# Kernel tuning notes

Hardware: AMD Instinct MI355X
Metric: run time of the kernel (lower is better)

## Reference

```python
import jax, jax.numpy as jnp
import numpy as np

WEIGHT_GROUP = 128  # in-channel group size for scales (module default)


def setup_inputs() -> dict:
    key = jax.random.key(0)
    k1, k2, k3, k4, k5 = jax.random.split(key, 5)
    B, IN, OUT = 16, 8192, 8192
    nG = IN // WEIGHT_GROUP  # 64 scale groups along in_features
    x = jax.random.normal(k1, (B, IN), dtype=jnp.float32)
    # 'weight' stores the already-quantized low-bit float values (small magnitudes)
    weight = jax.random.normal(k2, (OUT, IN), dtype=jnp.float32)
    # per-(row, group) positive scales
    scale_buf = jax.random.uniform(k3, (OUT, nG), dtype=jnp.float32, minval=0.01, maxval=1.0)
    bias = jax.random.normal(k4, (1, OUT), dtype=jnp.float32)
    # per-[64, group]-block mantissa-format ids in {0,1,2}; selects the dequant
    # format on hardware but is a constant lookup (no float math) in the reference
    types = jax.random.randint(k5, (OUT // 64, nG), 0, 3, dtype=jnp.int32)
    return {"x": x, "weight": weight, "scale_buf": scale_buf, "bias": bias, "types": types}


def reference(x, weight, scale_buf, bias, types):
    O, I = weight.shape
    nG = scale_buf.shape[1]
    G = I // nG
    # group-wise dequant: w_deq[o, g*G + j] = weight[o, g*G + j] * scale_buf[o, g]
    w_deq = (weight.reshape(O, nG, G) * scale_buf[:, :, None]).reshape(O, I)
    # y = x @ W_deq^T + bias   [B, O]
    return jnp.einsum("bi,oi->bo", x, w_deq) + bias
```

## Files before the change

### kernel.cpp

```cpp
#include <hip/hip_runtime.h>

#define IN_F 8192
#define OUT_F 8192
#define NBATCH 16
#define KC 512
#define NG 64

__global__ __launch_bounds__(256, 2)
void axcore_dsew_linear_kernel(const float* __restrict__ x,
                               const float* __restrict__ w,
                               const float* __restrict__ scale,
                               const float* __restrict__ bias,
                               float* __restrict__ out) {
    __shared__ __align__(16) float xlds[NBATCH * KC];

    const int t    = threadIdx.x;
    const int wv   = t >> 6;
    const int lane = t & 63;
    const int o0   = blockIdx.x * 16 + wv * 4;

    float acc[4][16];
#pragma unroll
    for (int r = 0; r < 4; ++r)
#pragma unroll
        for (int b = 0; b < NBATCH; ++b) acc[r][b] = 0.f;

    for (int kc = 0; kc < IN_F; kc += KC) {
        __syncthreads();
#pragma unroll
        for (int p = 0; p < 8; ++p) {
            const int fidx = p * 256 + t;
            const int bb = fidx >> 7;
            const int kq = fidx & 127;
            const float4 v = *(const float4*)&x[bb * IN_F + kc + 4 * kq];
            *(float4*)&xlds[bb * KC + 4 * kq] = v;
        }
        __syncthreads();

        float4 scq[4];
#pragma unroll
        for (int r = 0; r < 4; ++r)
            scq[r] = *(const float4*)&scale[(o0 + r) * NG + (kc >> 7)];

#pragma unroll
        for (int s = 0; s < 2; ++s) {
            const int klocal = s * 256 + 4 * lane;
            const int kg = kc + klocal;

            float4 wq[4];
#pragma unroll
            for (int r = 0; r < 4; ++r)
                wq[r] = *(const float4*)&w[(size_t)(o0 + r) * IN_F + kg];

#pragma unroll
            for (int r = 0; r < 4; ++r) {
                float sr;
                if (s == 0) sr = (lane < 32) ? scq[r].x : scq[r].y;
                else        sr = (lane < 32) ? scq[r].z : scq[r].w;
                wq[r].x *= sr; wq[r].y *= sr; wq[r].z *= sr; wq[r].w *= sr;
            }

#pragma unroll
            for (int b = 0; b < NBATCH; ++b) {
                const float4 xv = *(const float4*)&xlds[b * KC + klocal];
#pragma unroll
                for (int r = 0; r < 4; ++r) {
                    acc[r][b] += wq[r].x * xv.x;
                    acc[r][b] += wq[r].y * xv.y;
                    acc[r][b] += wq[r].z * xv.z;
                    acc[r][b] += wq[r].w * xv.w;
                }
            }
        }
    }

#pragma unroll
    for (int r = 0; r < 4; ++r) {
        const int o = o0 + r;
        const float bs = bias[o];
#pragma unroll
        for (int b = 0; b < NBATCH; ++b) {
            float v = acc[r][b];
            v += __shfl_xor(v, 1);
            v += __shfl_xor(v, 2);
            v += __shfl_xor(v, 4);
            v += __shfl_xor(v, 8);
            v += __shfl_xor(v, 16);
            v += __shfl_xor(v, 32);
            if (lane == 0) out[b * OUT_F + o] = v + bs;
        }
    }
}

extern "C" void kernel_launch(void* const* d_in, const int* in_sizes, int n_in,
                              void* d_out, int out_size, void* d_ws, size_t ws_size,
                              hipStream_t stream) {
    const float* x    = (const float*)d_in[0];
    const float* w    = (const float*)d_in[1];
    const float* sc   = (const float*)d_in[2];
    const float* bias = (const float*)d_in[3];
    float* out = (float*)d_out;

    dim3 grid(OUT_F / 16), block(256);
    hipLaunchKernelGGL(axcore_dsew_linear_kernel, grid, block, 0, stream,
                       x, w, sc, bias, out);
}
```

Before: 438.5 us.

## Split K across two blocks with atomic accumulation and prefetch weights before barrier

Splits the reduction dimension into two halves on a second grid axis. Partial sums are combined with atomicAdd into an output that a separate init kernel pre-fills with bias. The kernel also issues the weight and scale loads before the x staging and barrier so memory latency overlaps, and it raises the occupancy hint to four blocks per CU. The cost is an extra kernel launch, atomic traffic, and higher register pressure under the tighter launch bound.

```diff
diff --git a/kernel.cpp b/kernel.cpp
--- a/kernel.cpp
+++ b/kernel.cpp
@@ -5,70 +5,85 @@
 #define NBATCH 16
 #define KC 512
 #define NG 64
+#define KSPLIT 2
+#define KRANGE (IN_F / KSPLIT)
 
-__global__ __launch_bounds__(256, 2)
+__global__ __launch_bounds__(256)
+void init_out_kernel(const float* __restrict__ bias, float* __restrict__ out) {
+    const int i = blockIdx.x * 256 + threadIdx.x;
+    out[i] = bias[i & (OUT_F - 1)];
+}
+
+__global__ __launch_bounds__(256, 4)
 void axcore_dsew_linear_kernel(const float* __restrict__ x,
                                const float* __restrict__ w,
                                const float* __restrict__ scale,
-                               const float* __restrict__ bias,
                                float* __restrict__ out) {
     __shared__ __align__(16) float xlds[NBATCH * KC];
 
     const int t    = threadIdx.x;
-    const int wv   = t >> 6;
+    const int wv   = __builtin_amdgcn_readfirstlane(t >> 6);
     const int lane = t & 63;
     const int o0   = blockIdx.x * 16 + wv * 4;
+    const int k0   = blockIdx.y * KRANGE;
 
-    float acc[4][16];
+    float acc[4][NBATCH];
 #pragma unroll
     for (int r = 0; r < 4; ++r)
 #pragma unroll
         for (int b = 0; b < NBATCH; ++b) acc[r][b] = 0.f;
 
-    for (int kc = 0; kc < IN_F; kc += KC) {
+    for (int kc = k0; kc < k0 + KRANGE; kc += KC) {
         __syncthreads();
+
+        float4 wq[2][4];
+#pragma unroll
+        for (int s = 0; s < 2; ++s)
+#pragma unroll
+            for (int r = 0; r < 4; ++r)
+                wq[s][r] = *(const float4*)&w[(size_t)(o0 + r) * IN_F + kc + s * 256 + 4 * lane];
+
+        const int g0 = kc >> 7;
+        float sc[2][4];
+#pragma unroll
+        for (int s = 0; s < 2; ++s)
+#pragma unroll
+            for (int r = 0; r < 4; ++r) {
+                const float sa = scale[(o0 + r) * NG + g0 + 2 * s];
+                const float sb = scale[(o0 + r) * NG + g0 + 2 * s + 1];
+                sc[s][r] = (lane < 32) ? sa : sb;
+            }
+
 #pragma unroll
         for (int p = 0; p < 8; ++p) {
             const int fidx = p * 256 + t;
             const int bb = fidx >> 7;
             const int kq = fidx & 127;
-            const float4 v = *(const float4*)&x[bb * IN_F + kc + 4 * kq];
-            *(float4*)&xlds[bb * KC + 4 * kq] = v;
+            *(float4*)&xlds[bb * KC + 4 * kq] =
+                *(const float4*)&x[bb * IN_F + kc + 4 * kq];
         }
         __syncthreads();
-
-        float4 scq[4];
-#pragma unroll
-        for (int r = 0; r < 4; ++r)
-            scq[r] = *(const float4*)&scale[(o0 + r) * NG + (kc >> 7)];
 
 #pragma unroll
         for (int s = 0; s < 2; ++s) {
             const int klocal = s * 256 + 4 * lane;
-            const int kg = kc + klocal;
-
-            float4 wq[4];
-#pragma unroll
-            for (int r = 0; r < 4; ++r)
-                wq[r] = *(const float4*)&w[(size_t)(o0 + r) * IN_F + kg];
-
+            float4 wr[4];
 #pragma unroll
             for (int r = 0; r < 4; ++r) {
-                float sr;
-                if (s == 0) sr = (lane < 32) ? scq[r].x : scq[r].y;
-                else        sr = (lane < 32) ? scq[r].z : scq[r].w;
-                wq[r].x *= sr; wq[r].y *= sr; wq[r].z *= sr; wq[r].w *= sr;
+                wr[r].x = wq[s][r].x * sc[s][r];
+                wr[r].y = wq[s][r].y * sc[s][r];
+                wr[r].z = wq[s][r].z * sc[s][r];
+                wr[r].w = wq[s][r].w * sc[s][r];
             }
-
 #pragma unroll
             for (int b = 0; b < NBATCH; ++b) {
                 const float4 xv = *(const float4*)&xlds[b * KC + klocal];
 #pragma unroll
                 for (int r = 0; r < 4; ++r) {
-                    acc[r][b] += wq[r].x * xv.x;
-                    acc[r][b] += wq[r].y * xv.y;
-                    acc[r][b] += wq[r].z * xv.z;
-                    acc[r][b] += wq[r].w * xv.w;
+                    acc[r][b] += wr[r].x * xv.x;
+                    acc[r][b] += wr[r].y * xv.y;
+                    acc[r][b] += wr[r].z * xv.z;
+                    acc[r][b] += wr[r].w * xv.w;
                 }
             }
         }
@@ -77,7 +92,6 @@
 #pragma unroll
     for (int r = 0; r < 4; ++r) {
         const int o = o0 + r;
-        const float bs = bias[o];
 #pragma unroll
         for (int b = 0; b < NBATCH; ++b) {
             float v = acc[r][b];
@@ -87,7 +101,7 @@
             v += __shfl_xor(v, 8);
             v += __shfl_xor(v, 16);
             v += __shfl_xor(v, 32);
-            if (lane == 0) out[b * OUT_F + o] = v + bs;
+            if (lane == 0) atomicAdd(&out[b * OUT_F + o], v);
         }
     }
 }
@@ -101,7 +115,8 @@
     const float* bias = (const float*)d_in[3];
     float* out = (float*)d_out;
 
-    dim3 grid(OUT_F / 16), block(256);
-    hipLaunchKernelGGL(axcore_dsew_linear_kernel, grid, block, 0, stream,
-                       x, w, sc, bias, out);
+    hipLaunchKernelGGL(init_out_kernel, dim3(NBATCH * OUT_F / 256), dim3(256),
+                       0, stream, bias, out);
+    hipLaunchKernelGGL(axcore_dsew_linear_kernel, dim3(OUT_F / 16, KSPLIT), dim3(256),
+                       0, stream, x, w, sc, out);
 }
```

New measurement: 445.6 us. No clear change (+1.6%).
